# Kernel optimization log

Hardware: AMD Instinct MI355X
Metric: run time of the kernel (lower is better)

## Reference

```python
import jax, jax.numpy as jnp
import numpy as np

B, T, D, F, H = 512, 48, 128, 16, 512


def setup_inputs() -> dict:
    key = jax.random.key(0)
    ks = jax.random.split(key, 7)
    return {
        "input": jax.random.normal(ks[0], (B, T, D, F), dtype=jnp.float32),
        "attn_w": jax.random.normal(ks[1], (2 * H + F * T,), dtype=jnp.float32) * 0.02,
        "attn_b": jax.random.normal(ks[2], (1,), dtype=jnp.float32) * 0.02,
        "w_ih": jax.random.normal(ks[3], (4 * H, D * F), dtype=jnp.float32) * 0.02,
        "w_hh": jax.random.normal(ks[4], (4 * H, H), dtype=jnp.float32) * 0.02,
        "b_ih": jax.random.normal(ks[5], (4 * H,), dtype=jnp.float32) * 0.02,
        "b_hh": jax.random.normal(ks[6], (4 * H,), dtype=jnp.float32) * 0.02,
    }


def reference(input, attn_w, attn_b, w_ih, w_hh, b_ih, b_hh):
    Bsz, Ts, Dn, Fn = input.shape
    Hs = w_hh.shape[1]
    # permute(0,2,3,1): [B, T, D, F] -> [B, D, F, T]
    x_perm = jnp.transpose(input, (0, 2, 3, 1))
    x_flat = x_perm.reshape(Bsz, Dn, Fn * Ts)  # [B, D, F*T]
    # encode_attn input is concat(hidden, cell, x); split the weight accordingly
    w_h, w_c, w_x = attn_w[:Hs], attn_w[Hs:2 * Hs], attn_w[2 * Hs:]
    # x contribution to attention logits is constant across steps
    e_x = x_flat @ w_x + attn_b[0]             # [B, D]
    xs = jnp.moveaxis(x_perm, 3, 0)            # [T, B, D, F] (time-major for scan)
    bias = b_ih + b_hh                         # fuse the two LSTM biases

    def step(carry, x_t):
        h, c = carry                           # [B, H] each
        e = e_x + (h @ w_h)[:, None] + (c @ w_c)[:, None]  # [B, D]
        a = jax.nn.softmax(e, axis=-1)
        x_hat = (a[:, :, None] * x_t).reshape(Bsz, Dn * Fn)  # [B, D*F]
        gates = x_hat @ w_ih.T + h @ w_hh.T + bias            # [B, 4H]
        i, f, g, o = jnp.split(gates, 4, axis=-1)  # torch LSTM gate order
        c_new = jax.nn.sigmoid(f) * c + jax.nn.sigmoid(i) * jnp.tanh(g)
        h_new = jax.nn.sigmoid(o) * jnp.tanh(c_new)
        return (h_new, c_new), h_new

    h0 = jnp.zeros((Bsz, Hs), dtype=input.dtype)
    _, hs = jax.lax.scan(step, (h0, h0), xs)   # hs: [T, B, H]
    return jnp.transpose(hs, (1, 0, 2))        # [B, T, H] == hidden_states[:, 1:]
```

## Files before the change

### kernel.cpp

```cpp
#include <hip/hip_runtime.h>

#define B_ 512
#define T_ 48
#define D_ 128
#define F_ 16
#define H_ 512

typedef float f32x4 __attribute__((ext_vector_type(4)));
typedef short s16x8 __attribute__((ext_vector_type(8)));
typedef unsigned short u16x8 __attribute__((ext_vector_type(8)));
typedef unsigned short u16x4 __attribute__((ext_vector_type(4)));
typedef unsigned long long u64;

__device__ __forceinline__ unsigned short f2bf(float x) {
  unsigned u = __float_as_uint(x);
  u += 0x7fffu + ((u >> 16) & 1u);
  return (unsigned short)(u >> 16);
}
__device__ __forceinline__ float bf2f(unsigned short h) {
  return __uint_as_float(((unsigned)h) << 16);
}
__device__ __forceinline__ float sigmoidf_(float x) {
  return 1.f / (1.f + expf(-x));
}

__device__ __forceinline__ void st_sys_u64(u64* p, u64 v) {
  __hip_atomic_store(p, v, __ATOMIC_RELAXED, __HIP_MEMORY_SCOPE_SYSTEM);
}
__device__ __forceinline__ u64 ld_sys_u64(const u64* p) {
  return __hip_atomic_load((u64*)p, __ATOMIC_RELAXED, __HIP_MEMORY_SCOPE_SYSTEM);
}
__device__ __forceinline__ void st_sys_u32(unsigned* p, unsigned v) {
  __hip_atomic_store(p, v, __ATOMIC_RELAXED, __HIP_MEMORY_SCOPE_SYSTEM);
}
__device__ __forceinline__ unsigned ld_sys_u32(const unsigned* p) {
  return __hip_atomic_load((unsigned*)p, __ATOMIC_RELAXED, __HIP_MEMORY_SCOPE_SYSTEM);
}

#define AS1 __attribute__((address_space(1)))
#define AS3 __attribute__((address_space(3)))
__device__ __forceinline__ void g2lds16(const void* g, void* l) {
  __builtin_amdgcn_global_load_lds((const AS1 void*)g, (AS3 void*)l, 16, 0, 0);
}

__global__ __launch_bounds__(256) void k_prep(const float* __restrict__ wih,
                                              const float* __restrict__ whh,
                                              unsigned short* __restrict__ wih_b,
                                              unsigned short* __restrict__ whh_b) {
  long i4 = ((long)blockIdx.x * 256 + threadIdx.x) * 4;
  if (i4 < 4194304) {
    float4 v = *(const float4*)(wih + i4);
    u16x4 o = {f2bf(v.x), f2bf(v.y), f2bf(v.z), f2bf(v.w)};
    *(u16x4*)(wih_b + i4) = o;
  } else {
    long j = i4 - 4194304;
    if (j < 1048576) {
      float4 v = *(const float4*)(whh + j);
      u16x4 o = {f2bf(v.x), f2bf(v.y), f2bf(v.z), f2bf(v.w)};
      *(u16x4*)(whh_b + j) = o;
    }
  }
}

__global__ __launch_bounds__(128) void k_ex(const float* __restrict__ in,
                                            const float* __restrict__ attn_w,
                                            const float* __restrict__ attn_b,
                                            float* __restrict__ a_out) {
  __shared__ float wx[768];
  __shared__ float red[128];
  const int b = blockIdx.x, d = threadIdx.x;
  for (int i = d; i < 768; i += 128) wx[i] = attn_w[1024 + i];
  __syncthreads();
  const float* base = in + (long)b * 98304 + (long)d * 16;
  float acc = 0.f;
  for (int t = 0; t < 48; ++t) {
    const float4* p = (const float4*)(base + (long)t * 2048);
    float4 v0 = p[0], v1 = p[1], v2 = p[2], v3 = p[3];
    acc += v0.x * wx[t]       + v0.y * wx[48 + t]  + v0.z * wx[96 + t]  + v0.w * wx[144 + t];
    acc += v1.x * wx[192 + t] + v1.y * wx[240 + t] + v1.z * wx[288 + t] + v1.w * wx[336 + t];
    acc += v2.x * wx[384 + t] + v2.y * wx[432 + t] + v2.z * wx[480 + t] + v2.w * wx[528 + t];
    acc += v3.x * wx[576 + t] + v3.y * wx[624 + t] + v3.z * wx[672 + t] + v3.w * wx[720 + t];
  }
  acc += attn_b[0];
  red[d] = acc;
  __syncthreads();
  for (int s = 64; s > 0; s >>= 1) {
    if (d < s) red[d] = fmaxf(red[d], red[d + s]);
    __syncthreads();
  }
  float mx = red[0];
  __syncthreads();
  float ex = expf(acc - mx);
  red[d] = ex;
  __syncthreads();
  for (int s = 64; s > 0; s >>= 1) {
    if (d < s) red[d] += red[d + s];
    __syncthreads();
  }
  a_out[b * 128 + d] = ex / red[0];
}

__global__ __launch_bounds__(256) void k_xhat(const float* __restrict__ in,
                                              const float* __restrict__ a,
                                              unsigned short* __restrict__ xh) {
  const int mrow = blockIdx.x;
  const int t = mrow >> 9, b = mrow & 511;
  const int tid = threadIdx.x;
  const int k = tid * 8;
  const int d = k >> 4;
  const int f0 = k & 15;
  const float* src = in + (((long)(b * 48 + t) * 128 + d) * 16 + f0);
  float4 v0 = *(const float4*)src;
  float4 v1 = *(const float4*)(src + 4);
  float s = a[b * 128 + d];
  u16x8 o;
  o[0] = f2bf(v0.x * s); o[1] = f2bf(v0.y * s); o[2] = f2bf(v0.z * s); o[3] = f2bf(v0.w * s);
  o[4] = f2bf(v1.x * s); o[5] = f2bf(v1.y * s); o[6] = f2bf(v1.z * s); o[7] = f2bf(v1.w * s);
  *(u16x8*)(xh + (long)mrow * 2048 + k) = o;
}


#define G_STAGE(ktv, s)                                                         \
  do {                                                                          \
    const long ko_ = (long)(ktv) * 64 + (long)(s) * 262144;                     \
    char* la_ = (char*)SM + ((ktv) & 1) * 32768 + (s) * 16384 + ldsw;           \
    g2lds16(Ag + ko_, la_);                                                     \
    g2lds16(Ag + ko_ + 131072, la_ + 8192);                                     \
    g2lds16(Bg + ko_, la_ + 65536);                                             \
    g2lds16(Bg + ko_ + 131072, la_ + 73728);                                    \
  } while (0)

#define G_LDA4(dst, bufel, ksv, mh)                                             \
  do {                                                                          \
    const unsigned short* ab_ =                                                 \
        SM + (bufel) + aBase + (mh) * 4096 + (psw ^ ((ksv) * 32));              \
    dst[0] = *(const s16x8*)(ab_);                                              \
    dst[1] = *(const s16x8*)(ab_ + 1024);                                       \
    dst[2] = *(const s16x8*)(ab_ + 2048);                                       \
    dst[3] = *(const s16x8*)(ab_ + 3072);                                       \
  } while (0)

#define G_LDB4(dst, bufel, ksv)                                                 \
  do {                                                                          \
    const unsigned short* bb_ = SM + (bufel) + bBase + (psw ^ ((ksv) * 32));    \
    dst[0] = *(const s16x8*)(bb_);                                              \
    dst[1] = *(const s16x8*)(bb_ + 1024);                                       \
    dst[2] = *(const s16x8*)(bb_ + 2048);                                       \
    dst[3] = *(const s16x8*)(bb_ + 3072);                                       \
  } while (0)

#define G_MMA2(mh, Af, Bf)                                                      \
  do {                                                                          \
    __builtin_amdgcn_s_setprio(1);                                              \
    _Pragma("unroll") for (int mt_ = 0; mt_ < 4; ++mt_)                         \
        _Pragma("unroll") for (int nt_ = 0; nt_ < 4; ++nt_)                     \
            acc[(mh) * 4 + mt_][nt_] = __builtin_amdgcn_mfma_f32_16x16x32_bf16( \
                Af[mt_], Bf[nt_], acc[(mh) * 4 + mt_][nt_], 0, 0, 0);           \
    __builtin_amdgcn_s_setprio(0);                                              \
  } while (0)

#define G_GATE(n) asm volatile("s_waitcnt vmcnt(" #n ")" ::: "memory")

__global__ __launch_bounds__(512, 2) void k_gemm(const unsigned short* __restrict__ A,
                                                 const unsigned short* __restrict__ Bw,
                                                 unsigned short* __restrict__ C) {
  __shared__ __align__(16) unsigned short SM[65536];
  const int tid = threadIdx.x;
  const int w = tid >> 6, lane = tid & 63;
  const int q = lane >> 4, l16 = lane & 15;
  const int wm = w >> 2, wn = w & 3;
  const int id = blockIdx.x;
  const int xcd = id & 7, j = id >> 3;
  const long m0 = ((long)xcd * 12 + (j >> 3)) * 256;
  const long n0 = (long)(j & 7) * 256;

  const int srow = w * 8 + (lane >> 3);
  const int csrc = (lane & 7) ^ (lane >> 3);
  const unsigned short* Ag = A + (m0 + srow) * 2048 + csrc * 8;
  const unsigned short* Bg = Bw + (n0 + srow) * 2048 + csrc * 8;
  const int ldsw = w * 1024;

  const int psw = (q ^ (l16 & 7)) * 8;
  const int aBase = (wm * 128 + l16) * 64;
  const int bBase = 32768 + (wn * 64 + l16) * 64;

  f32x4 acc[8][4];
  const f32x4 zz = {0.f, 0.f, 0.f, 0.f};
#pragma unroll
  for (int i = 0; i < 8; ++i)
#pragma unroll
    for (int j2 = 0; j2 < 4; ++j2) acc[i][j2] = zz;

  G_STAGE(0, 0);
  G_STAGE(0, 1);
  G_GATE(0);
  __builtin_amdgcn_s_barrier();

#pragma unroll 1
  for (int kt = 0; kt < 31; ++kt) {
    const int bufel = (kt & 1) * 16384;
    s16x8 b0[4], b1[4], a00[4], a01[4], a10[4], a11[4];
    G_LDB4(b0, bufel, 0);
    G_LDA4(a00, bufel, 0, 0);
    G_STAGE(kt + 1, 0);
    G_LDA4(a01, bufel, 0, 1);
    G_STAGE(kt + 1, 1);
    G_MMA2(0, a00, b0);
    G_LDB4(b1, bufel, 1);
    G_LDA4(a10, bufel, 1, 0);
    G_MMA2(1, a01, b0);
    G_LDA4(a11, bufel, 1, 1);
    G_MMA2(0, a10, b1);
    G_MMA2(1, a11, b1);
    G_GATE(0);
    __builtin_amdgcn_s_barrier();
  }
  {
    s16x8 b0[4], b1[4], a00[4], a01[4], a10[4], a11[4];
    G_LDB4(b0, 16384, 0);
    G_LDA4(a00, 16384, 0, 0);
    G_LDA4(a01, 16384, 0, 1);
    G_MMA2(0, a00, b0);
    G_LDB4(b1, 16384, 1);
    G_LDA4(a10, 16384, 1, 0);
    G_MMA2(1, a01, b0);
    G_LDA4(a11, 16384, 1, 1);
    G_MMA2(0, a10, b1);
    G_MMA2(1, a11, b1);
  }

#pragma unroll
  for (int mh = 0; mh < 2; ++mh)
#pragma unroll
    for (int mt = 0; mt < 4; ++mt)
#pragma unroll
      for (int nt = 0; nt < 4; ++nt)
#pragma unroll
        for (int r = 0; r < 4; ++r) {
          long m = m0 + wm * 128 + mh * 64 + mt * 16 + q * 4 + r;
          long n = n0 + wn * 64 + nt * 16 + l16;
          C[m * 2048 + n] = f2bf(acc[mh * 4 + mt][nt][r]);
        }
}

__global__ __launch_bounds__(256, 1) void k_rec(const unsigned short* __restrict__ gx,
                                                const unsigned short* __restrict__ whh_b,
                                                const float* __restrict__ b_ih,
                                                const float* __restrict__ b_hh,
                                                unsigned short* __restrict__ h_buf,
                                                float* __restrict__ out,
                                                unsigned int* __restrict__ bar) {
  __shared__ unsigned short hs[32 * 520];
  __shared__ float gsm[4 * 32 * 37];
  const int tid = threadIdx.x;
  const int wave = tid >> 6, lane = tid & 63;
  const int q = lane >> 4, l16 = lane & 15;
  const int bt = blockIdx.x & 15, g = blockIdx.x >> 4;
  const int b0 = bt * 32;
  const int pm = tid >> 3, pr = (tid & 7) * 4;
  const int srow = tid >> 3, st7 = tid & 7;
  unsigned int* slots = &bar[bt * 16];

  s16x8 wreg[32];
#pragma unroll
  for (int nt = 0; nt < 2; ++nt) {
    const unsigned short* wp = whh_b + (long)(wave * 512 + g * 32 + nt * 16 + l16) * 512 + q * 8;
#pragma unroll
    for (int kk = 0; kk < 16; ++kk)
      wreg[nt * 16 + kk] = *(const s16x8*)(wp + kk * 32);
  }
#pragma unroll
  for (int i = 0; i < 32; ++i) asm volatile("" : "+v"(wreg[i]));

  float bias_[16];
#pragma unroll
  for (int qq = 0; qq < 4; ++qq)
#pragma unroll
    for (int rr = 0; rr < 4; ++rr) {
      int j = qq * 512 + g * 32 + pr + rr;
      bias_[qq * 4 + rr] = b_ih[j] + b_hh[j];
    }
  float creg[4] = {0.f, 0.f, 0.f, 0.f};
  const f32x4 zz = {0.f, 0.f, 0.f, 0.f};

  for (int t = 0; t < 48; ++t) {
    u16x4 gxr[4];
    const unsigned short* gp = gx + ((long)t * 512 + b0 + pm) * 2048 + g * 32 + pr;
#pragma unroll
    for (int qq = 0; qq < 4; ++qq) gxr[qq] = *(const u16x4*)(gp + qq * 512);

    f32x4 acc[2][2] = {{zz, zz}, {zz, zz}};
    if (t > 0) {
      if (wave == 0 && lane < 16) {
        while (ld_sys_u32(&slots[lane]) < (unsigned)t)
          __builtin_amdgcn_s_sleep(1);
      }
      __syncthreads();
      const u64* hp = (const u64*)(h_buf + ((t - 1) & 1) * (512 * 512) + (long)b0 * 512);
      u64 tmp[16];
#pragma unroll
      for (int j = 0; j < 16; ++j)
        tmp[j] = ld_sys_u64(hp + (long)srow * 128 + st7 + 8 * j);
#pragma unroll
      for (int j = 0; j < 16; ++j)
        *(u64*)&hs[srow * 520 + (st7 + 8 * j) * 4] = tmp[j];
      __syncthreads();
#pragma unroll
      for (int kk = 0; kk < 16; ++kk) {
        s16x8 af0 = *(const s16x8*)&hs[l16 * 520 + kk * 32 + q * 8];
        s16x8 af1 = *(const s16x8*)&hs[(16 + l16) * 520 + kk * 32 + q * 8];
        acc[0][0] = __builtin_amdgcn_mfma_f32_16x16x32_bf16(af0, wreg[kk],      acc[0][0], 0, 0, 0);
        acc[0][1] = __builtin_amdgcn_mfma_f32_16x16x32_bf16(af0, wreg[16 + kk], acc[0][1], 0, 0, 0);
        acc[1][0] = __builtin_amdgcn_mfma_f32_16x16x32_bf16(af1, wreg[kk],      acc[1][0], 0, 0, 0);
        acc[1][1] = __builtin_amdgcn_mfma_f32_16x16x32_bf16(af1, wreg[16 + kk], acc[1][1], 0, 0, 0);
      }
    }
#pragma unroll
    for (int mt = 0; mt < 2; ++mt)
#pragma unroll
      for (int nt = 0; nt < 2; ++nt)
        *(f32x4*)&gsm[(wave * 32 + nt * 16 + l16) * 37 + mt * 16 + q * 4] = acc[mt][nt];
    __syncthreads();
    float hval[4];
#pragma unroll
    for (int rr = 0; rr < 4; ++rr) {
      float gv[4];
#pragma unroll
      for (int qq = 0; qq < 4; ++qq)
        gv[qq] = gsm[(qq * 32 + pr + rr) * 37 + pm] + bf2f(gxr[qq][rr]) + bias_[qq * 4 + rr];
      float is = sigmoidf_(gv[0]);
      float fs = sigmoidf_(gv[1]);
      float gt = tanhf(gv[2]);
      float os = sigmoidf_(gv[3]);
      creg[rr] = fs * creg[rr] + is * gt;
      hval[rr] = os * tanhf(creg[rr]);
    }
    u16x4 hb = {f2bf(hval[0]), f2bf(hval[1]), f2bf(hval[2]), f2bf(hval[3])};
    u64 hb8;
    __builtin_memcpy(&hb8, &hb, 8);
    st_sys_u64((u64*)&h_buf[(t & 1) * (512 * 512) + (b0 + pm) * 512 + g * 32 + pr], hb8);
    __syncthreads();
    if (t < 47 && tid == 0)
      st_sys_u32(&slots[g], (unsigned)(t + 1));
    f32x4 ov = {hval[0], hval[1], hval[2], hval[3]};
    __builtin_nontemporal_store(ov, (f32x4*)&out[(long)(b0 + pm) * (T_ * H_) + (long)t * H_ + g * 32 + pr]);
  }
}

extern "C" void kernel_launch(void* const* d_in, const int* in_sizes, int n_in,
                              void* d_out, int out_size, void* d_ws, size_t ws_size,
                              hipStream_t stream) {
  const float* input  = (const float*)d_in[0];
  const float* attn_w = (const float*)d_in[1];
  const float* attn_b = (const float*)d_in[2];
  const float* w_ih   = (const float*)d_in[3];
  const float* w_hh   = (const float*)d_in[4];
  const float* b_ih   = (const float*)d_in[5];
  const float* b_hh   = (const float*)d_in[6];
  float* out = (float*)d_out;

  char* ws = (char*)d_ws;
  unsigned int* bar     = (unsigned int*)ws;
  float* a_ws           = (float*)(ws + 1024);
  unsigned short* h_buf = (unsigned short*)(ws + 263168);
  unsigned short* whh_b = (unsigned short*)(ws + 1311744);
  unsigned short* wih_b = (unsigned short*)(ws + 3408896);
  unsigned short* x_hat = (unsigned short*)(ws + 11797504);
  unsigned short* gxws  = (unsigned short*)(ws + 112460800);

  (void)hipMemsetAsync(d_ws, 0, 1024, stream);
  hipLaunchKernelGGL(k_prep, dim3(5120), dim3(256), 0, stream, w_ih, w_hh, wih_b, whh_b);
  hipLaunchKernelGGL(k_ex, dim3(512), dim3(128), 0, stream, input, attn_w, attn_b, a_ws);
  hipLaunchKernelGGL(k_xhat, dim3(24576), dim3(256), 0, stream, input, a_ws, x_hat);
  hipLaunchKernelGGL(k_gemm, dim3(768), dim3(512), 0, stream, x_hat, wih_b, gxws);
  hipLaunchKernelGGL(k_rec, dim3(256), dim3(256), 0, stream, gxws, whh_b, b_ih, b_hh, h_buf, out, bar);
}
```

Before: 718.4 us.

## Restructure GEMM B loads to registers and split recurrent LSTM K across waves

The input-projection GEMM now loads B (weight) fragments straight from global memory into double-buffered registers and stages only A through LDS, which halves shared memory and drops the B LDS round trip. The recurrent kernel splits the hidden-state K dimension across waves, so each wave waits only on the 4 producer slots it needs and streams h chunks from global into registers, reading the block's own chunk from local LDS. It then reduces the partial sums through an LDS slab. Sigmoid and tanh use hardware exp2/rcp intrinsics. Gate and h stores change to per-element 16-bit layouts, which adds more narrow global stores and a larger LDS reduction.

```diff
diff --git a/kernel.cpp b/kernel.cpp
--- a/kernel.cpp
+++ b/kernel.cpp
@@ -20,8 +20,13 @@
 __device__ __forceinline__ float bf2f(unsigned short h) {
   return __uint_as_float(((unsigned)h) << 16);
 }
-__device__ __forceinline__ float sigmoidf_(float x) {
-  return 1.f / (1.f + expf(-x));
+__device__ __forceinline__ float fsig(float x) {
+  float e = __builtin_amdgcn_exp2f(-1.442695041f * x);
+  return __builtin_amdgcn_rcpf(1.f + e);
+}
+__device__ __forceinline__ float ftanh(float x) {
+  float e = __builtin_amdgcn_exp2f(2.885390082f * x);
+  return 1.f - 2.f * __builtin_amdgcn_rcpf(1.f + e);
 }
 
 __device__ __forceinline__ void st_sys_u64(u64* p, u64 v) {
@@ -29,6 +34,9 @@
 }
 __device__ __forceinline__ u64 ld_sys_u64(const u64* p) {
   return __hip_atomic_load((u64*)p, __ATOMIC_RELAXED, __HIP_MEMORY_SCOPE_SYSTEM);
+}
+__device__ __forceinline__ void st_sys_u16(unsigned short* p, unsigned short v) {
+  __hip_atomic_store(p, v, __ATOMIC_RELAXED, __HIP_MEMORY_SCOPE_SYSTEM);
 }
 __device__ __forceinline__ void st_sys_u32(unsigned* p, unsigned v) {
   __hip_atomic_store(p, v, __ATOMIC_RELAXED, __HIP_MEMORY_SCOPE_SYSTEM);
@@ -119,15 +127,12 @@
   *(u16x8*)(xh + (long)mrow * 2048 + k) = o;
 }
 
-
-#define G_STAGE(ktv, s)                                                         \
+#define G_STAGEA(ktv, s)                                                        \
   do {                                                                          \
     const long ko_ = (long)(ktv) * 64 + (long)(s) * 262144;                     \
     char* la_ = (char*)SM + ((ktv) & 1) * 32768 + (s) * 16384 + ldsw;           \
     g2lds16(Ag + ko_, la_);                                                     \
     g2lds16(Ag + ko_ + 131072, la_ + 8192);                                     \
-    g2lds16(Bg + ko_, la_ + 65536);                                             \
-    g2lds16(Bg + ko_ + 131072, la_ + 73728);                                    \
   } while (0)
 
 #define G_LDA4(dst, bufel, ksv, mh)                                             \
@@ -140,31 +145,49 @@
     dst[3] = *(const s16x8*)(ab_ + 3072);                                       \
   } while (0)
 
-#define G_LDB4(dst, bufel, ksv)                                                 \
-  do {                                                                          \
-    const unsigned short* bb_ = SM + (bufel) + bBase + (psw ^ ((ksv) * 32));    \
-    dst[0] = *(const s16x8*)(bb_);                                              \
-    dst[1] = *(const s16x8*)(bb_ + 1024);                                       \
-    dst[2] = *(const s16x8*)(bb_ + 2048);                                       \
-    dst[3] = *(const s16x8*)(bb_ + 3072);                                       \
-  } while (0)
-
-#define G_MMA2(mh, Af, Bf)                                                      \
+#define G_LDBG(dst, ktv)                                                        \
+  do {                                                                          \
+    const unsigned short* bp_ = Bg + (long)(ktv) * 64;                          \
+    _Pragma("unroll") for (int nt_ = 0; nt_ < 4; ++nt_)                         \
+        _Pragma("unroll") for (int ks_ = 0; ks_ < 2; ++ks_)                     \
+            dst[nt_][ks_] = *(const s16x8*)(bp_ + nt_ * 16 * 2048 + ks_ * 32);  \
+  } while (0)
+
+#define G_MMA2(mh, Af, BC, ksv)                                                 \
   do {                                                                          \
     __builtin_amdgcn_s_setprio(1);                                              \
     _Pragma("unroll") for (int mt_ = 0; mt_ < 4; ++mt_)                         \
         _Pragma("unroll") for (int nt_ = 0; nt_ < 4; ++nt_)                     \
             acc[(mh) * 4 + mt_][nt_] = __builtin_amdgcn_mfma_f32_16x16x32_bf16( \
-                Af[mt_], Bf[nt_], acc[(mh) * 4 + mt_][nt_], 0, 0, 0);           \
+                Af[mt_], BC[nt_][ksv], acc[(mh) * 4 + mt_][nt_], 0, 0, 0);      \
     __builtin_amdgcn_s_setprio(0);                                              \
   } while (0)
 
 #define G_GATE(n) asm volatile("s_waitcnt vmcnt(" #n ")" ::: "memory")
+
+#define G_TILE(ktv, BC, BN)                                                     \
+  do {                                                                          \
+    const int bufel_ = ((ktv) & 1) * 16384;                                     \
+    s16x8 a0[4], a1[4];                                                         \
+    G_LDBG(BN, (ktv) + 1);                                                      \
+    G_LDA4(a0, bufel_, 0, 0);                                                   \
+    G_STAGEA((ktv) + 1, 0);                                                     \
+    G_STAGEA((ktv) + 1, 1);                                                     \
+    G_MMA2(0, a0, BC, 0);                                                       \
+    G_LDA4(a1, bufel_, 0, 1);                                                   \
+    G_MMA2(1, a1, BC, 0);                                                       \
+    G_LDA4(a0, bufel_, 1, 0);                                                   \
+    G_MMA2(0, a0, BC, 1);                                                       \
+    G_LDA4(a1, bufel_, 1, 1);                                                   \
+    G_MMA2(1, a1, BC, 1);                                                       \
+    G_GATE(0);                                                                  \
+    __builtin_amdgcn_s_barrier();                                               \
+  } while (0)
 
 __global__ __launch_bounds__(512, 2) void k_gemm(const unsigned short* __restrict__ A,
                                                  const unsigned short* __restrict__ Bw,
                                                  unsigned short* __restrict__ C) {
-  __shared__ __align__(16) unsigned short SM[65536];
+  __shared__ __align__(16) unsigned short SM[32768];
   const int tid = threadIdx.x;
   const int w = tid >> 6, lane = tid & 63;
   const int q = lane >> 4, l16 = lane & 15;
@@ -177,12 +200,12 @@
   const int srow = w * 8 + (lane >> 3);
   const int csrc = (lane & 7) ^ (lane >> 3);
   const unsigned short* Ag = A + (m0 + srow) * 2048 + csrc * 8;
-  const unsigned short* Bg = Bw + (n0 + srow) * 2048 + csrc * 8;
   const int ldsw = w * 1024;
+
+  const unsigned short* Bg = Bw + (n0 + wn * 64 + l16) * 2048 + q * 8;
 
   const int psw = (q ^ (l16 & 7)) * 8;
   const int aBase = (wm * 128 + l16) * 64;
-  const int bBase = 32768 + (wn * 64 + l16) * 64;
 
   f32x4 acc[8][4];
   const f32x4 zz = {0.f, 0.f, 0.f, 0.f};
@@ -191,42 +214,30 @@
 #pragma unroll
     for (int j2 = 0; j2 < 4; ++j2) acc[i][j2] = zz;
 
-  G_STAGE(0, 0);
-  G_STAGE(0, 1);
+  s16x8 bA[4][2], bB[4][2];
+  G_LDBG(bA, 0);
+  G_STAGEA(0, 0);
+  G_STAGEA(0, 1);
   G_GATE(0);
   __builtin_amdgcn_s_barrier();
 
 #pragma unroll 1
-  for (int kt = 0; kt < 31; ++kt) {
-    const int bufel = (kt & 1) * 16384;
-    s16x8 b0[4], b1[4], a00[4], a01[4], a10[4], a11[4];
-    G_LDB4(b0, bufel, 0);
-    G_LDA4(a00, bufel, 0, 0);
-    G_STAGE(kt + 1, 0);
-    G_LDA4(a01, bufel, 0, 1);
-    G_STAGE(kt + 1, 1);
-    G_MMA2(0, a00, b0);
-    G_LDB4(b1, bufel, 1);
-    G_LDA4(a10, bufel, 1, 0);
-    G_MMA2(1, a01, b0);
-    G_LDA4(a11, bufel, 1, 1);
-    G_MMA2(0, a10, b1);
-    G_MMA2(1, a11, b1);
-    G_GATE(0);
-    __builtin_amdgcn_s_barrier();
-  }
+  for (int kt2 = 0; kt2 < 15; ++kt2) {
+    const int kt = kt2 * 2;
+    G_TILE(kt, bA, bB);
+    G_TILE(kt + 1, bB, bA);
+  }
+  G_TILE(30, bA, bB);
   {
-    s16x8 b0[4], b1[4], a00[4], a01[4], a10[4], a11[4];
-    G_LDB4(b0, 16384, 0);
-    G_LDA4(a00, 16384, 0, 0);
-    G_LDA4(a01, 16384, 0, 1);
-    G_MMA2(0, a00, b0);
-    G_LDB4(b1, 16384, 1);
-    G_LDA4(a10, 16384, 1, 0);
-    G_MMA2(1, a01, b0);
-    G_LDA4(a11, 16384, 1, 1);
-    G_MMA2(0, a10, b1);
-    G_MMA2(1, a11, b1);
+    s16x8 a0[4], a1[4];
+    G_LDA4(a0, 16384, 0, 0);
+    G_MMA2(0, a0, bB, 0);
+    G_LDA4(a1, 16384, 0, 1);
+    G_MMA2(1, a1, bB, 0);
+    G_LDA4(a0, 16384, 1, 0);
+    G_MMA2(0, a0, bB, 1);
+    G_LDA4(a1, 16384, 1, 1);
+    G_MMA2(1, a1, bB, 1);
   }
 
 #pragma unroll
@@ -250,101 +261,158 @@
                                                 unsigned short* __restrict__ h_buf,
                                                 float* __restrict__ out,
                                                 unsigned int* __restrict__ bar) {
-  __shared__ unsigned short hs[32 * 520];
-  __shared__ float gsm[4 * 32 * 37];
+  __shared__ __align__(16) float slab[16 * 32 * 36];
+  __shared__ __align__(16) unsigned short hs_own[32 * 40];
   const int tid = threadIdx.x;
-  const int wave = tid >> 6, lane = tid & 63;
+  const int w = tid >> 6, lane = tid & 63;
   const int q = lane >> 4, l16 = lane & 15;
   const int bt = blockIdx.x & 15, g = blockIdx.x >> 4;
   const int b0 = bt * 32;
-  const int pm = tid >> 3, pr = (tid & 7) * 4;
-  const int srow = tid >> 3, st7 = tid & 7;
+  const int pj = tid & 31;
+  const int pr0 = (tid >> 5) * 4;
   unsigned int* slots = &bar[bt * 16];
+  const int ownw = ((g >> 2) == w);
+  const int ownc = g & 3;
 
   s16x8 wreg[32];
 #pragma unroll
-  for (int nt = 0; nt < 2; ++nt) {
-    const unsigned short* wp = whh_b + (long)(wave * 512 + g * 32 + nt * 16 + l16) * 512 + q * 8;
-#pragma unroll
-    for (int kk = 0; kk < 16; ++kk)
-      wreg[nt * 16 + kk] = *(const s16x8*)(wp + kk * 32);
-  }
-#pragma unroll
-  for (int i = 0; i < 32; ++i) asm volatile("" : "+v"(wreg[i]));
-
-  float bias_[16];
-#pragma unroll
-  for (int qq = 0; qq < 4; ++qq)
-#pragma unroll
-    for (int rr = 0; rr < 4; ++rr) {
-      int j = qq * 512 + g * 32 + pr + rr;
-      bias_[qq * 4 + rr] = b_ih[j] + b_hh[j];
-    }
+  for (int quad = 0; quad < 4; ++quad)
+#pragma unroll
+    for (int nt = 0; nt < 2; ++nt)
+#pragma unroll
+      for (int ci = 0; ci < 4; ++ci) {
+        const unsigned short* wp =
+            whh_b + (long)(quad * 512 + g * 32 + nt * 16 + l16) * 512 + (w * 4 + ci) * 32 + q * 8;
+        asm volatile("global_load_dwordx4 %0, %1, off"
+                     : "=v"(wreg[(quad * 2 + nt) * 4 + ci]) : "v"(wp) : "memory");
+      }
+  asm volatile("s_waitcnt vmcnt(0)" ::: "memory");
+  __builtin_amdgcn_sched_barrier(0);
+
+  float bias_[4];
+#pragma unroll
+  for (int qq = 0; qq < 4; ++qq) {
+    int jj = qq * 512 + g * 32 + pj;
+    bias_[qq] = b_ih[jj] + b_hh[jj];
+  }
   float creg[4] = {0.f, 0.f, 0.f, 0.f};
   const f32x4 zz = {0.f, 0.f, 0.f, 0.f};
 
+#define LD_CHUNK(slot, ci)                                                      \
+  do {                                                                          \
+    long o_ = hbase + (w * 4 + (ci)) * 8;                                       \
+    L[slot][0] = ld_sys_u64(hb + o_);                                           \
+    L[slot][1] = ld_sys_u64(hb + o_ + 1);                                       \
+    L[slot][2] = ld_sys_u64(hb + o_ + 2048);                                    \
+    L[slot][3] = ld_sys_u64(hb + o_ + 2049);                                    \
+  } while (0)
+
   for (int t = 0; t < 48; ++t) {
-    u16x4 gxr[4];
-    const unsigned short* gp = gx + ((long)t * 512 + b0 + pm) * 2048 + g * 32 + pr;
-#pragma unroll
-    for (int qq = 0; qq < 4; ++qq) gxr[qq] = *(const u16x4*)(gp + qq * 512);
-
-    f32x4 acc[2][2] = {{zz, zz}, {zz, zz}};
+    unsigned short gxr[4][4];
+    const unsigned short* gp = gx + ((long)t * 512 + b0 + pr0) * 2048 + g * 32 + pj;
+#pragma unroll
+    for (int rr = 0; rr < 4; ++rr)
+#pragma unroll
+      for (int qq = 0; qq < 4; ++qq)
+        gxr[qq][rr] = gp[rr * 2048 + qq * 512];
+
     if (t > 0) {
-      if (wave == 0 && lane < 16) {
-        while (ld_sys_u32(&slots[lane]) < (unsigned)t)
-          __builtin_amdgcn_s_sleep(1);
+      const int need = (lane < 4) && !(ownw && lane == ownc);
+      const unsigned* fp = &slots[w * 4 + (lane & 3)];
+      while (1) {
+        unsigned v = need ? ld_sys_u32(fp) : 0xffffffffu;
+        if (__all((int)(v >= (unsigned)t))) break;
       }
-      __syncthreads();
-      const u64* hp = (const u64*)(h_buf + ((t - 1) & 1) * (512 * 512) + (long)b0 * 512);
-      u64 tmp[16];
-#pragma unroll
-      for (int j = 0; j < 16; ++j)
-        tmp[j] = ld_sys_u64(hp + (long)srow * 128 + st7 + 8 * j);
-#pragma unroll
-      for (int j = 0; j < 16; ++j)
-        *(u64*)&hs[srow * 520 + (st7 + 8 * j) * 4] = tmp[j];
-      __syncthreads();
-#pragma unroll
-      for (int kk = 0; kk < 16; ++kk) {
-        s16x8 af0 = *(const s16x8*)&hs[l16 * 520 + kk * 32 + q * 8];
-        s16x8 af1 = *(const s16x8*)&hs[(16 + l16) * 520 + kk * 32 + q * 8];
-        acc[0][0] = __builtin_amdgcn_mfma_f32_16x16x32_bf16(af0, wreg[kk],      acc[0][0], 0, 0, 0);
-        acc[0][1] = __builtin_amdgcn_mfma_f32_16x16x32_bf16(af0, wreg[16 + kk], acc[0][1], 0, 0, 0);
-        acc[1][0] = __builtin_amdgcn_mfma_f32_16x16x32_bf16(af1, wreg[kk],      acc[1][0], 0, 0, 0);
-        acc[1][1] = __builtin_amdgcn_mfma_f32_16x16x32_bf16(af1, wreg[16 + kk], acc[1][1], 0, 0, 0);
+      u64 L[2][4];
+      const u64* hb = (const u64*)(h_buf + ((t - 1) & 1) * (512 * 512));
+      const long hbase = (long)(b0 + l16) * 128 + q * 2;
+      f32x4 acc[4][2][2];
+#pragma unroll
+      for (int a = 0; a < 4; ++a)
+#pragma unroll
+        for (int b = 0; b < 2; ++b)
+#pragma unroll
+          for (int c = 0; c < 2; ++c) acc[a][b][c] = zz;
+      if (!(ownw && 0 == ownc)) LD_CHUNK(0, 0);
+#pragma unroll
+      for (int ci = 0; ci < 4; ++ci) {
+        if (ci < 3 && !(ownw && (ci + 1) == ownc)) LD_CHUNK((ci + 1) & 1, ci + 1);
+        s16x8 af0, af1;
+        if (ownw && ci == ownc) {
+          af0 = *(const s16x8*)&hs_own[l16 * 40 + q * 8];
+          af1 = *(const s16x8*)&hs_own[(16 + l16) * 40 + q * 8];
+        } else {
+          union { u64 u[2]; s16x8 v; } c0, c1;
+          c0.u[0] = L[ci & 1][0]; c0.u[1] = L[ci & 1][1];
+          c1.u[0] = L[ci & 1][2]; c1.u[1] = L[ci & 1][3];
+          af0 = c0.v; af1 = c1.v;
+        }
+#pragma unroll
+        for (int quad = 0; quad < 4; ++quad)
+#pragma unroll
+          for (int nt = 0; nt < 2; ++nt) {
+            acc[quad][nt][0] = __builtin_amdgcn_mfma_f32_16x16x32_bf16(
+                af0, wreg[(quad * 2 + nt) * 4 + ci], acc[quad][nt][0], 0, 0, 0);
+            acc[quad][nt][1] = __builtin_amdgcn_mfma_f32_16x16x32_bf16(
+                af1, wreg[(quad * 2 + nt) * 4 + ci], acc[quad][nt][1], 0, 0, 0);
+          }
+      }
+#pragma unroll
+      for (int quad = 0; quad < 4; ++quad)
+#pragma unroll
+        for (int nt = 0; nt < 2; ++nt)
+#pragma unroll
+          for (int mh = 0; mh < 2; ++mh)
+            *(f32x4*)&slab[((w * 4 + quad) * 32 + nt * 16 + l16) * 36 + mh * 16 + q * 4] =
+                acc[quad][nt][mh];
+    }
+    __syncthreads();
+
+    float hval[4];
+    {
+      f32x4 gs[4];
+      if (t > 0) {
+#pragma unroll
+        for (int qq = 0; qq < 4; ++qq) {
+          f32x4 s0 = *(const f32x4*)&slab[((0 * 4 + qq) * 32 + pj) * 36 + pr0];
+          f32x4 s1 = *(const f32x4*)&slab[((1 * 4 + qq) * 32 + pj) * 36 + pr0];
+          f32x4 s2 = *(const f32x4*)&slab[((2 * 4 + qq) * 32 + pj) * 36 + pr0];
+          f32x4 s3 = *(const f32x4*)&slab[((3 * 4 + qq) * 32 + pj) * 36 + pr0];
+          gs[qq] = (s0 + s1) + (s2 + s3);
+        }
+      } else {
+#pragma unroll
+        for (int qq = 0; qq < 4; ++qq) gs[qq] = zz;
+      }
+#pragma unroll
+      for (int rr = 0; rr < 4; ++rr) {
+        float g0 = gs[0][rr] + bias_[0] + bf2f(gxr[0][rr]);
+        float g1 = gs[1][rr] + bias_[1] + bf2f(gxr[1][rr]);
+        float g2 = gs[2][rr] + bias_[2] + bf2f(gxr[2][rr]);
+        float g3 = gs[3][rr] + bias_[3] + bf2f(gxr[3][rr]);
+        float is = fsig(g0);
+        float fs = fsig(g1);
+        float gt = ftanh(g2);
+        float os = fsig(g3);
+        creg[rr] = fs * creg[rr] + is * gt;
+        hval[rr] = os * ftanh(creg[rr]);
       }
     }
 #pragma unroll
-    for (int mt = 0; mt < 2; ++mt)
-#pragma unroll
-      for (int nt = 0; nt < 2; ++nt)
-        *(f32x4*)&gsm[(wave * 32 + nt * 16 + l16) * 37 + mt * 16 + q * 4] = acc[mt][nt];
-    __syncthreads();
-    float hval[4];
-#pragma unroll
     for (int rr = 0; rr < 4; ++rr) {
-      float gv[4];
-#pragma unroll
-      for (int qq = 0; qq < 4; ++qq)
-        gv[qq] = gsm[(qq * 32 + pr + rr) * 37 + pm] + bf2f(gxr[qq][rr]) + bias_[qq * 4 + rr];
-      float is = sigmoidf_(gv[0]);
-      float fs = sigmoidf_(gv[1]);
-      float gt = tanhf(gv[2]);
-      float os = sigmoidf_(gv[3]);
-      creg[rr] = fs * creg[rr] + is * gt;
-      hval[rr] = os * tanhf(creg[rr]);
+      unsigned short hb16 = f2bf(hval[rr]);
+      hs_own[(pr0 + rr) * 40 + pj] = hb16;
+      st_sys_u16(&h_buf[(t & 1) * (512 * 512) + (b0 + pr0 + rr) * 512 + g * 32 + pj], hb16);
     }
-    u16x4 hb = {f2bf(hval[0]), f2bf(hval[1]), f2bf(hval[2]), f2bf(hval[3])};
-    u64 hb8;
-    __builtin_memcpy(&hb8, &hb, 8);
-    st_sys_u64((u64*)&h_buf[(t & 1) * (512 * 512) + (b0 + pm) * 512 + g * 32 + pr], hb8);
     __syncthreads();
     if (t < 47 && tid == 0)
       st_sys_u32(&slots[g], (unsigned)(t + 1));
-    f32x4 ov = {hval[0], hval[1], hval[2], hval[3]};
-    __builtin_nontemporal_store(ov, (f32x4*)&out[(long)(b0 + pm) * (T_ * H_) + (long)t * H_ + g * 32 + pr]);
-  }
+#pragma unroll
+    for (int rr = 0; rr < 4; ++rr)
+      __builtin_nontemporal_store(
+          hval[rr], &out[(long)(b0 + pr0 + rr) * (T_ * H_) + (long)t * H_ + g * 32 + pj]);
+  }
+#undef LD_CHUNK
 }
 
 extern "C" void kernel_launch(void* const* d_in, const int* in_sizes, int n_in,
```

New measurement: 852.1 us. 1.19x slower.

## Split attention logit kernel, prefetch GEMM fragments, swizzle recurrent LDS, fast activations

Applied to the files above, without the earlier changes.

The attention logit kernel is split into a partial-sum kernel over four time chunks with 2048 blocks, plus a reduce/softmax kernel, to raise parallelism on the input read. The GEMM main loop now prefetches the first A/B LDS fragments of the next k-tile before the last MMA group, overlapping LDS reads with compute. The recurrent kernel replaces padded LDS rows with an XOR swizzle and loads its weights with inline asm. Sigmoid and tanh use hardware exp2/rcp intrinsics, which cut latency on the serial recurrence at some cost in accuracy. The changes also add an extra kernel launch.

```diff
diff --git a/kernel.cpp b/kernel.cpp
--- a/kernel.cpp
+++ b/kernel.cpp
@@ -20,8 +20,13 @@
 __device__ __forceinline__ float bf2f(unsigned short h) {
   return __uint_as_float(((unsigned)h) << 16);
 }
-__device__ __forceinline__ float sigmoidf_(float x) {
-  return 1.f / (1.f + expf(-x));
+__device__ __forceinline__ float fsig(float x) {
+  float e = __builtin_amdgcn_exp2f(-1.442695041f * x);
+  return __builtin_amdgcn_rcpf(1.f + e);
+}
+__device__ __forceinline__ float ftanh(float x) {
+  float e = __builtin_amdgcn_exp2f(2.885390082f * x);
+  return 1.f - 2.f * __builtin_amdgcn_rcpf(1.f + e);
 }
 
 __device__ __forceinline__ void st_sys_u64(u64* p, u64 v) {
@@ -62,26 +67,36 @@
   }
 }
 
-__global__ __launch_bounds__(128) void k_ex(const float* __restrict__ in,
-                                            const float* __restrict__ attn_w,
-                                            const float* __restrict__ attn_b,
-                                            float* __restrict__ a_out) {
+__global__ __launch_bounds__(256) void k_ex1(const float* __restrict__ in,
+                                             const float* __restrict__ attn_w,
+                                             float* __restrict__ e_part) {
   __shared__ float wx[768];
+  const int bc = blockIdx.x;
+  const int b = bc >> 2, c = bc & 3;
+  const int tid = threadIdx.x;
+  const int d = tid >> 1, fh = tid & 1;
+  for (int i = tid; i < 768; i += 256) wx[i] = attn_w[1024 + i];
+  __syncthreads();
+  const float* base = in + (long)b * 98304 + (long)d * 16 + fh * 8;
+  float acc = 0.f;
+  for (int t = c * 12; t < c * 12 + 12; ++t) {
+    const float4* p = (const float4*)(base + (long)t * 2048);
+    float4 v0 = p[0], v1 = p[1];
+    const float* wt = wx + fh * 384 + t;
+    acc += v0.x * wt[0]   + v0.y * wt[48]  + v0.z * wt[96]  + v0.w * wt[144];
+    acc += v1.x * wt[192] + v1.y * wt[240] + v1.z * wt[288] + v1.w * wt[336];
+  }
+  acc += __shfl_xor(acc, 1);
+  if (fh == 0) e_part[(long)bc * 128 + d] = acc;
+}
+
+__global__ __launch_bounds__(128) void k_ex2(const float* __restrict__ e_part,
+                                             const float* __restrict__ attn_b,
+                                             float* __restrict__ a_out) {
   __shared__ float red[128];
   const int b = blockIdx.x, d = threadIdx.x;
-  for (int i = d; i < 768; i += 128) wx[i] = attn_w[1024 + i];
-  __syncthreads();
-  const float* base = in + (long)b * 98304 + (long)d * 16;
-  float acc = 0.f;
-  for (int t = 0; t < 48; ++t) {
-    const float4* p = (const float4*)(base + (long)t * 2048);
-    float4 v0 = p[0], v1 = p[1], v2 = p[2], v3 = p[3];
-    acc += v0.x * wx[t]       + v0.y * wx[48 + t]  + v0.z * wx[96 + t]  + v0.w * wx[144 + t];
-    acc += v1.x * wx[192 + t] + v1.y * wx[240 + t] + v1.z * wx[288 + t] + v1.w * wx[336 + t];
-    acc += v2.x * wx[384 + t] + v2.y * wx[432 + t] + v2.z * wx[480 + t] + v2.w * wx[528 + t];
-    acc += v3.x * wx[576 + t] + v3.y * wx[624 + t] + v3.z * wx[672 + t] + v3.w * wx[720 + t];
-  }
-  acc += attn_b[0];
+  float acc = attn_b[0];
+  for (int c = 0; c < 4; ++c) acc += e_part[(long)(b * 4 + c) * 128 + d];
   red[d] = acc;
   __syncthreads();
   for (int s = 64; s > 0; s >>= 1) {
@@ -159,8 +174,6 @@
     __builtin_amdgcn_s_setprio(0);                                              \
   } while (0)
 
-#define G_GATE(n) asm volatile("s_waitcnt vmcnt(" #n ")" ::: "memory")
-
 __global__ __launch_bounds__(512, 2) void k_gemm(const unsigned short* __restrict__ A,
                                                  const unsigned short* __restrict__ Bw,
                                                  unsigned short* __restrict__ C) {
@@ -191,41 +204,42 @@
 #pragma unroll
     for (int j2 = 0; j2 < 4; ++j2) acc[i][j2] = zz;
 
+  s16x8 na0[4], nb0[4];
   G_STAGE(0, 0);
   G_STAGE(0, 1);
-  G_GATE(0);
+  asm volatile("s_waitcnt vmcnt(0)" ::: "memory");
   __builtin_amdgcn_s_barrier();
+  G_LDB4(nb0, 0, 0);
+  G_LDA4(na0, 0, 0, 0);
 
 #pragma unroll 1
   for (int kt = 0; kt < 31; ++kt) {
     const int bufel = (kt & 1) * 16384;
-    s16x8 b0[4], b1[4], a00[4], a01[4], a10[4], a11[4];
-    G_LDB4(b0, bufel, 0);
-    G_LDA4(a00, bufel, 0, 0);
+    s16x8 b1[4], a01[4], a10[4], a11[4];
     G_STAGE(kt + 1, 0);
+    G_STAGE(kt + 1, 1);
+    G_MMA2(0, na0, nb0);
     G_LDA4(a01, bufel, 0, 1);
-    G_STAGE(kt + 1, 1);
-    G_MMA2(0, a00, b0);
+    G_MMA2(1, a01, nb0);
     G_LDB4(b1, bufel, 1);
     G_LDA4(a10, bufel, 1, 0);
-    G_MMA2(1, a01, b0);
+    G_MMA2(0, a10, b1);
     G_LDA4(a11, bufel, 1, 1);
-    G_MMA2(0, a10, b1);
+    asm volatile("s_waitcnt vmcnt(0) lgkmcnt(0)" ::: "memory");
+    __builtin_amdgcn_s_barrier();
+    G_LDB4(nb0, bufel ^ 16384, 0);
+    G_LDA4(na0, bufel ^ 16384, 0, 0);
     G_MMA2(1, a11, b1);
-    G_GATE(0);
-    __builtin_amdgcn_s_barrier();
   }
   {
-    s16x8 b0[4], b1[4], a00[4], a01[4], a10[4], a11[4];
-    G_LDB4(b0, 16384, 0);
-    G_LDA4(a00, 16384, 0, 0);
+    s16x8 b1[4], a01[4], a10[4], a11[4];
+    G_MMA2(0, na0, nb0);
     G_LDA4(a01, 16384, 0, 1);
-    G_MMA2(0, a00, b0);
+    G_MMA2(1, a01, nb0);
     G_LDB4(b1, 16384, 1);
     G_LDA4(a10, 16384, 1, 0);
-    G_MMA2(1, a01, b0);
+    G_MMA2(0, a10, b1);
     G_LDA4(a11, 16384, 1, 1);
-    G_MMA2(0, a10, b1);
     G_MMA2(1, a11, b1);
   }
 
@@ -250,7 +264,7 @@
                                                 unsigned short* __restrict__ h_buf,
                                                 float* __restrict__ out,
                                                 unsigned int* __restrict__ bar) {
-  __shared__ unsigned short hs[32 * 520];
+  __shared__ __align__(16) unsigned short hs[32 * 512];
   __shared__ float gsm[4 * 32 * 37];
   const int tid = threadIdx.x;
   const int wave = tid >> 6, lane = tid & 63;
@@ -259,26 +273,30 @@
   const int b0 = bt * 32;
   const int pm = tid >> 3, pr = (tid & 7) * 4;
   const int srow = tid >> 3, st7 = tid & 7;
+  const int sxk = srow & 7;
+  const int rxk = l16 & 7;
   unsigned int* slots = &bar[bt * 16];
 
   s16x8 wreg[32];
 #pragma unroll
-  for (int nt = 0; nt < 2; ++nt) {
-    const unsigned short* wp = whh_b + (long)(wave * 512 + g * 32 + nt * 16 + l16) * 512 + q * 8;
-#pragma unroll
-    for (int kk = 0; kk < 16; ++kk)
-      wreg[nt * 16 + kk] = *(const s16x8*)(wp + kk * 32);
-  }
-#pragma unroll
-  for (int i = 0; i < 32; ++i) asm volatile("" : "+v"(wreg[i]));
+  for (int nt = 0; nt < 2; ++nt)
+#pragma unroll
+    for (int kk = 0; kk < 16; ++kk) {
+      const unsigned short* wp =
+          whh_b + (long)(wave * 512 + g * 32 + nt * 16 + l16) * 512 + kk * 32 + q * 8;
+      asm volatile("global_load_dwordx4 %0, %1, off"
+                   : "=v"(wreg[nt * 16 + kk]) : "v"(wp) : "memory");
+    }
+  asm volatile("s_waitcnt vmcnt(0)" ::: "memory");
+  __builtin_amdgcn_sched_barrier(0);
 
   float bias_[16];
 #pragma unroll
   for (int qq = 0; qq < 4; ++qq)
 #pragma unroll
     for (int rr = 0; rr < 4; ++rr) {
-      int j = qq * 512 + g * 32 + pr + rr;
-      bias_[qq * 4 + rr] = b_ih[j] + b_hh[j];
+      int jj = qq * 512 + g * 32 + pr + rr;
+      bias_[qq * 4 + rr] = b_ih[jj] + b_hh[jj];
     }
   float creg[4] = {0.f, 0.f, 0.f, 0.f};
   const f32x4 zz = {0.f, 0.f, 0.f, 0.f};
@@ -302,13 +320,17 @@
       for (int j = 0; j < 16; ++j)
         tmp[j] = ld_sys_u64(hp + (long)srow * 128 + st7 + 8 * j);
 #pragma unroll
-      for (int j = 0; j < 16; ++j)
-        *(u64*)&hs[srow * 520 + (st7 + 8 * j) * 4] = tmp[j];
+      for (int j = 0; j < 16; ++j) {
+        const int idx = st7 + 8 * j;
+        const int c = idx >> 1, half = idx & 1;
+        *(u64*)&hs[srow * 512 + ((c ^ sxk) << 3) + (half << 2)] = tmp[j];
+      }
       __syncthreads();
 #pragma unroll
       for (int kk = 0; kk < 16; ++kk) {
-        s16x8 af0 = *(const s16x8*)&hs[l16 * 520 + kk * 32 + q * 8];
-        s16x8 af1 = *(const s16x8*)&hs[(16 + l16) * 520 + kk * 32 + q * 8];
+        const int c = 4 * kk + q;
+        s16x8 af0 = *(const s16x8*)&hs[l16 * 512 + ((c ^ rxk) << 3)];
+        s16x8 af1 = *(const s16x8*)&hs[(16 + l16) * 512 + ((c ^ rxk) << 3)];
         acc[0][0] = __builtin_amdgcn_mfma_f32_16x16x32_bf16(af0, wreg[kk],      acc[0][0], 0, 0, 0);
         acc[0][1] = __builtin_amdgcn_mfma_f32_16x16x32_bf16(af0, wreg[16 + kk], acc[0][1], 0, 0, 0);
         acc[1][0] = __builtin_amdgcn_mfma_f32_16x16x32_bf16(af1, wreg[kk],      acc[1][0], 0, 0, 0);
@@ -328,12 +350,12 @@
 #pragma unroll
       for (int qq = 0; qq < 4; ++qq)
         gv[qq] = gsm[(qq * 32 + pr + rr) * 37 + pm] + bf2f(gxr[qq][rr]) + bias_[qq * 4 + rr];
-      float is = sigmoidf_(gv[0]);
-      float fs = sigmoidf_(gv[1]);
-      float gt = tanhf(gv[2]);
-      float os = sigmoidf_(gv[3]);
+      float is = fsig(gv[0]);
+      float fs = fsig(gv[1]);
+      float gt = ftanh(gv[2]);
+      float os = fsig(gv[3]);
       creg[rr] = fs * creg[rr] + is * gt;
-      hval[rr] = os * tanhf(creg[rr]);
+      hval[rr] = os * ftanh(creg[rr]);
     }
     u16x4 hb = {f2bf(hval[0]), f2bf(hval[1]), f2bf(hval[2]), f2bf(hval[3])};
     u64 hb8;
@@ -367,10 +389,12 @@
   unsigned short* wih_b = (unsigned short*)(ws + 3408896);
   unsigned short* x_hat = (unsigned short*)(ws + 11797504);
   unsigned short* gxws  = (unsigned short*)(ws + 112460800);
+  float* e_part         = (float*)x_hat;
 
   (void)hipMemsetAsync(d_ws, 0, 1024, stream);
   hipLaunchKernelGGL(k_prep, dim3(5120), dim3(256), 0, stream, w_ih, w_hh, wih_b, whh_b);
-  hipLaunchKernelGGL(k_ex, dim3(512), dim3(128), 0, stream, input, attn_w, attn_b, a_ws);
+  hipLaunchKernelGGL(k_ex1, dim3(2048), dim3(256), 0, stream, input, attn_w, e_part);
+  hipLaunchKernelGGL(k_ex2, dim3(512), dim3(128), 0, stream, e_part, attn_b, a_ws);
   hipLaunchKernelGGL(k_xhat, dim3(24576), dim3(256), 0, stream, input, a_ws, x_hat);
   hipLaunchKernelGGL(k_gemm, dim3(768), dim3(512), 0, stream, x_hat, wih_b, gxws);
   hipLaunchKernelGGL(k_rec, dim3(256), dim3(256), 0, stream, gxws, whh_b, b_ih, b_hh, h_buf, out, bar);
```

Result: faster. 701.7 us (-2.3%).
